# Kernel optimization log

Hardware: AMD Instinct MI355X
Metric: run time of the kernel (lower is better)

The kernel has to match this reference:

```python
import jax, jax.numpy as jnp
import numpy as np

N_NODES = 50000
N_EDGES = 1600000
IN_CH = 128
HEADS = 4
HEAD_DIM = 32  # out_channels // heads = 128 // 4
NEG_SLOPE = 0.2


def setup_inputs() -> dict:
    key = jax.random.key(0)
    ks = jax.random.split(key, 6)
    x = jax.random.normal(ks[0], (N_NODES, IN_CH), dtype=jnp.float32)
    edge_index = jax.random.randint(ks[1], (2, N_EDGES), 0, N_NODES, dtype=jnp.int64)
    W = jax.random.normal(ks[2], (IN_CH, HEADS * HEAD_DIM), dtype=jnp.float32) * 0.1
    att_src = jax.random.normal(ks[3], (HEADS, HEAD_DIM), dtype=jnp.float32) * 0.1
    att_dst = jax.random.normal(ks[4], (HEADS, HEAD_DIM), dtype=jnp.float32) * 0.1
    bias = jax.random.normal(ks[5], (HEADS * HEAD_DIM,), dtype=jnp.float32) * 0.1
    return {"x": x, "edge_index": edge_index, "W": W,
            "att_src": att_src, "att_dst": att_dst, "bias": bias}


def reference(x, edge_index, W, att_src, att_dst, bias):
    N = x.shape[0]
    # linear projection, split heads: [N, H, C]
    h = (x @ W).reshape(N, HEADS, HEAD_DIM)
    # per-node attention logits: [N, H]
    a_src = jnp.einsum('nhc,hc->nh', h, att_src)
    a_dst = jnp.einsum('nhc,hc->nh', h, att_dst)
    # add self loops (PyG default)
    loops = jnp.arange(N, dtype=edge_index.dtype)
    src = jnp.concatenate([edge_index[0], loops])  # message source j
    dst = jnp.concatenate([edge_index[1], loops])  # message target i
    # edge attention scores: [E_total, H]
    alpha = jax.nn.leaky_relu(a_src[src] + a_dst[dst], NEG_SLOPE)
    # segment softmax over incoming edges per destination node
    amax = jax.ops.segment_max(alpha, dst, num_segments=N)
    alpha = jnp.exp(alpha - amax[dst])
    denom = jax.ops.segment_sum(alpha, dst, num_segments=N)
    alpha = alpha / (denom[dst] + 1e-16)
    # weighted scatter-aggregate: [N, H, C]
    msg = h[src] * alpha[:, :, None]
    out = jax.ops.segment_sum(msg, dst, num_segments=N)
    out = out.reshape(N, HEADS * HEAD_DIM) + bias
    return jax.nn.elu(out)
```

## Files before the change

### kernel.cpp

```cpp
#include <hip/hip_runtime.h>

typedef unsigned short u16;
typedef unsigned int u32;

#define CH 128
#define NHEAD 4
#define NEG_SLOPE 0.2f
#define ROWS_PER_BLOCK 32

#define LOG_NPB 7
#define NPB 128
#define NBMAX 400
#define BCAP 6144
#define KMAX 24
#define GPAD 16
#define BINA_BLOCKS 256

static __device__ __forceinline__ float bitf(u32 i) {
    float f; __builtin_memcpy(&f, &i, 4); return f;
}
static __device__ __forceinline__ float bflo(u32 v) { return bitf(v << 16); }
static __device__ __forceinline__ float bfhi(u32 v) { return bitf(v & 0xffff0000u); }
static __device__ __forceinline__ u16 f2bf(float f) {
    u32 i; __builtin_memcpy(&i, &f, 4);
    return (u16)((i + 0x7fffu + ((i >> 16) & 1u)) >> 16);
}
static __device__ __forceinline__ float lrelu(float v) { return v > 0.f ? v : NEG_SLOPE * v; }

static __device__ __forceinline__ int ei_at(const int* __restrict__ ei, int mode32, size_t idx) {
    return mode32 ? ei[idx] : ei[2 * idx];
}

__global__ __launch_bounds__(256) void gemmbin_kernel(
    const float* __restrict__ x, const float* __restrict__ W,
    const float* __restrict__ att_src, const float* __restrict__ att_dst,
    u16* __restrict__ h, float* __restrict__ asrc, float* __restrict__ adst, int N,
    const int* __restrict__ ei, int* __restrict__ gcur, u32* __restrict__ rec,
    int E, int NB)
{
    __shared__ float xs[ROWS_PER_BLOCK][CH];
    __shared__ u32 Wbf[CH][CH / 2];

    const int tid = threadIdx.x;

    if (blockIdx.x < BINA_BLOCKS) {
        int* hist  = (int*)&xs[0][0];
        int* hbase = hist + NBMAX;
        int* hcur  = hbase + NBMAX;
        const int mode32 = __syncthreads_or(ei[2 * tid + 1] != 0);
        for (int b = tid; b < NB; b += 256) { hist[b] = 0; hcur[b] = 0; }
        __syncthreads();
        const int chunk = (E + BINA_BLOCKS - 1) / BINA_BLOCKS;
        const int beg0 = blockIdx.x * chunk;
        const int end0 = min(E, beg0 + chunk);
#pragma unroll 4
        for (int e = beg0 + tid; e < end0; e += 256) {
            int dj = ei_at(ei, mode32, (size_t)E + e);
            atomicAdd(&hist[dj >> LOG_NPB], 1);
        }
        __syncthreads();
        for (int b = tid; b < NB; b += 256) {
            int c = hist[b];
            hbase[b] = c ? atomicAdd(&gcur[b * GPAD], c) : 0;
        }
        __syncthreads();
#pragma unroll 4
        for (int e = beg0 + tid; e < end0; e += 256) {
            int dj = ei_at(ei, mode32, (size_t)E + e);
            int sj = ei_at(ei, mode32, (size_t)e);
            int bkt = dj >> LOG_NPB;
            int r = atomicAdd(&hcur[bkt], 1);
            int pos = hbase[bkt] + r;
            if (pos < BCAP)
                rec[(size_t)bkt * BCAP + pos] = ((u32)sj << LOG_NPB) | (u32)(dj & (NPB - 1));
        }
        return;
    }

    const int gb = blockIdx.x - BINA_BLOCKS;
    const int r0b = gb * ROWS_PER_BLOCK;
    {
#pragma unroll
        for (int i = 0; i < 16; ++i) {
            int f = tid + i * 256;
            int row = f >> 5;
            int col = (f & 31) * 4;
            float4 w4 = *(const float4*)(W + (size_t)row * CH + col);
            Wbf[row][(col >> 1)]     = (u32)f2bf(w4.x) | ((u32)f2bf(w4.y) << 16);
            Wbf[row][(col >> 1) + 1] = (u32)f2bf(w4.z) | ((u32)f2bf(w4.w) << 16);
        }
#pragma unroll
        for (int i = 0; i < 4; ++i) {
            int f = tid + i * 256;
            int row = f >> 5;
            int col = (f & 31) * 4;
            if (r0b + row < N)
                *(float4*)&xs[row][col] = *(const float4*)(x + (size_t)(r0b + row) * CH + col);
        }
    }
    __syncthreads();

    const int lane = tid & 63;
    const int wave = tid >> 6;
    const int c0 = lane * 2;
    const int head = lane >> 4;
    const float as0 = att_src[c0], as1 = att_src[c0 + 1];
    const float ad0 = att_dst[c0], ad1 = att_dst[c0 + 1];
    const int rw = wave * 8;

    float acc[8][2];
#pragma unroll
    for (int r = 0; r < 8; ++r) { acc[r][0] = 0.f; acc[r][1] = 0.f; }

#pragma unroll 4
    for (int k4 = 0; k4 < 32; ++k4) {
        const int k = k4 * 4;
        u32 p0 = Wbf[k + 0][lane];
        u32 p1 = Wbf[k + 1][lane];
        u32 p2 = Wbf[k + 2][lane];
        u32 p3 = Wbf[k + 3][lane];
        float w00 = bflo(p0), w01 = bfhi(p0);
        float w10 = bflo(p1), w11 = bfhi(p1);
        float w20 = bflo(p2), w21 = bfhi(p2);
        float w30 = bflo(p3), w31 = bfhi(p3);
#pragma unroll
        for (int r = 0; r < 8; ++r) {
            float4 xv = *(const float4*)&xs[rw + r][k];
            acc[r][0] = fmaf(xv.x, w00, acc[r][0]);
            acc[r][1] = fmaf(xv.x, w01, acc[r][1]);
            acc[r][0] = fmaf(xv.y, w10, acc[r][0]);
            acc[r][1] = fmaf(xv.y, w11, acc[r][1]);
            acc[r][0] = fmaf(xv.z, w20, acc[r][0]);
            acc[r][1] = fmaf(xv.z, w21, acc[r][1]);
            acc[r][0] = fmaf(xv.w, w30, acc[r][0]);
            acc[r][1] = fmaf(xv.w, w31, acc[r][1]);
        }
    }
#pragma unroll
    for (int r = 0; r < 8; ++r) {
        int row = r0b + rw + r;
        float sdot = acc[r][0] * as0 + acc[r][1] * as1;
        float ddot = acc[r][0] * ad0 + acc[r][1] * ad1;
#pragma unroll
        for (int o = 1; o < 16; o <<= 1) {
            sdot += __shfl_xor(sdot, o, 64);
            ddot += __shfl_xor(ddot, o, 64);
        }
        if (row < N) {
            u32 hp = (u32)f2bf(acc[r][0]) | ((u32)f2bf(acc[r][1]) << 16);
            *(u32*)(h + (size_t)row * CH + c0) = hp;
            if ((lane & 15) == 0) {
                asrc[row * NHEAD + head] = sdot;
                adst[row * NHEAD + head] = ddot;
            }
        }
    }
}

__global__ __launch_bounds__(256) void binB_kernel(
    const int* __restrict__ gcur, const u32* __restrict__ rec,
    int* __restrict__ csr, int* __restrict__ begA, int* __restrict__ degA, int N)
{
    __shared__ int outb[BCAP];
    __shared__ int lcnt[NPB];
    __shared__ int lsc[NPB];
    __shared__ int lcur[NPB];
    const int tid = threadIdx.x;
    const int bkt = blockIdx.x;
    int cnt0 = gcur[bkt * GPAD];
    cnt0 = cnt0 < BCAP ? cnt0 : BCAP;
    const size_t rbase = (size_t)bkt * BCAP;

    if (tid < NPB) { lcnt[tid] = 0; lcur[tid] = 0; }

    u32 rc[KMAX];
#pragma unroll
    for (int k = 0; k < KMAX; ++k) {
        int i = tid + k * 256;
        rc[k] = (i < cnt0) ? rec[rbase + i] : 0xffffffffu;
    }
    __syncthreads();
#pragma unroll
    for (int k = 0; k < KMAX; ++k)
        if (rc[k] != 0xffffffffu) atomicAdd(&lcnt[rc[k] & (NPB - 1)], 1);
    __syncthreads();
    if (tid < NPB) lsc[tid] = lcnt[tid];
    __syncthreads();
    for (int o = 1; o < NPB; o <<= 1) {
        int v = (tid < NPB && tid >= o) ? lsc[tid - o] : 0;
        __syncthreads();
        if (tid < NPB) lsc[tid] += v;
        __syncthreads();
    }
#pragma unroll
    for (int k = 0; k < KMAX; ++k) {
        if (rc[k] != 0xffffffffu) {
            int local = rc[k] & (NPB - 1);
            int r = atomicAdd(&lcur[local], 1);
            int slot = (lsc[local] - lcnt[local]) + r;
            outb[slot] = (int)(rc[k] >> LOG_NPB);
        }
    }
    __syncthreads();
    for (int i = tid; i < cnt0; i += 256)
        csr[rbase + i] = outb[i];
    if (tid < NPB) {
        int node = (bkt << LOG_NPB) + tid;
        if (node < N) {
            begA[node] = (int)rbase + (lsc[tid] - lcnt[tid]);
            degA[node] = lcnt[tid];
        }
    }
}

__global__ __launch_bounds__(256) void agg_kernel(
    const u16* __restrict__ h, const float* __restrict__ asrc, const float* __restrict__ adst,
    const int* __restrict__ begA, const int* __restrict__ degA, const int* __restrict__ csr,
    const float* __restrict__ bias, float* __restrict__ out, int N)
{
    const int lane = threadIdx.x & 63;
    const int wave = threadIdx.x >> 6;
    const int node = blockIdx.x * 4 + wave;
    if (node >= N) return;
    const int g = lane >> 4;
    const int l = lane & 15;
    const int c8 = l * 8;
    const int head = l >> 2;
    const int beg = begA[node];
    const int end = beg + degA[node];
    const float4 ad4 = *(const float4*)(adst + node * 4);
    const float adh = (head == 0) ? ad4.x : (head == 1) ? ad4.y : (head == 2) ? ad4.z : ad4.w;
    const float4 asl = *(const float4*)(asrc + node * 4);
    const float aslh = (head == 0) ? asl.x : (head == 1) ? asl.y : (head == 2) ? asl.z : asl.w;
    const float mh = lrelu(aslh + adh);

    float acc[8];
#pragma unroll
    for (int k = 0; k < 8; ++k) acc[k] = 0.f;
    float s = 0.f;

    int e = beg + g;
    if (e < end) {
        int j0 = csr[e];
        int j1 = csr[e + 4];
        bool v1 = (e + 4) < end;
        j0 = ((u32)j0 < (u32)N) ? j0 : 0;
        j1 = ((u32)j1 < (u32)N) ? j1 : 0;
        float a0 = asrc[j0 * NHEAD + head];
        float a1 = asrc[j1 * NHEAD + head];
        a1 = v1 ? a1 : -1e30f;
        uint4 h0 = *(const uint4*)(h + (size_t)j0 * CH + c8);
        uint4 h1 = *(const uint4*)(h + (size_t)j1 * CH + c8);
        for (;;) {
            const int ep = e + 8;
            bool vp0 = ep < end;
            bool vp1 = (ep + 4) < end;
            int jp0 = csr[ep];
            int jp1 = csr[ep + 4];
            jp0 = ((u32)jp0 < (u32)N) ? jp0 : 0;
            jp1 = ((u32)jp1 < (u32)N) ? jp1 : 0;
            float ap0 = asrc[jp0 * NHEAD + head];
            float ap1 = asrc[jp1 * NHEAD + head];
            ap0 = vp0 ? ap0 : -1e30f;
            ap1 = vp1 ? ap1 : -1e30f;
            uint4 hp0 = *(const uint4*)(h + (size_t)jp0 * CH + c8);
            uint4 hp1 = *(const uint4*)(h + (size_t)jp1 * CH + c8);

            float w0 = __expf(lrelu(a0 + adh) - mh);
            float w1 = __expf(lrelu(a1 + adh) - mh);
            s += w0 + w1;
            acc[0] = fmaf(w0, bflo(h0.x), acc[0]);
            acc[1] = fmaf(w0, bfhi(h0.x), acc[1]);
            acc[2] = fmaf(w0, bflo(h0.y), acc[2]);
            acc[3] = fmaf(w0, bfhi(h0.y), acc[3]);
            acc[4] = fmaf(w0, bflo(h0.z), acc[4]);
            acc[5] = fmaf(w0, bfhi(h0.z), acc[5]);
            acc[6] = fmaf(w0, bflo(h0.w), acc[6]);
            acc[7] = fmaf(w0, bfhi(h0.w), acc[7]);
            acc[0] = fmaf(w1, bflo(h1.x), acc[0]);
            acc[1] = fmaf(w1, bfhi(h1.x), acc[1]);
            acc[2] = fmaf(w1, bflo(h1.y), acc[2]);
            acc[3] = fmaf(w1, bfhi(h1.y), acc[3]);
            acc[4] = fmaf(w1, bflo(h1.z), acc[4]);
            acc[5] = fmaf(w1, bfhi(h1.z), acc[5]);
            acc[6] = fmaf(w1, bflo(h1.w), acc[6]);
            acc[7] = fmaf(w1, bfhi(h1.w), acc[7]);

            a0 = ap0; a1 = ap1; h0 = hp0; h1 = hp1; e = ep;
            if (e >= end) break;
        }
    }
    if (g == 0) {
        s += 1.0f;
        uint4 hv = *(const uint4*)(h + (size_t)node * CH + c8);
        acc[0] += bflo(hv.x);
        acc[1] += bfhi(hv.x);
        acc[2] += bflo(hv.y);
        acc[3] += bfhi(hv.y);
        acc[4] += bflo(hv.z);
        acc[5] += bfhi(hv.z);
        acc[6] += bflo(hv.w);
        acc[7] += bfhi(hv.w);
    }
#pragma unroll
    for (int o = 16; o < 64; o <<= 1) {
        s += __shfl_xor(s, o, 64);
#pragma unroll
        for (int k = 0; k < 8; ++k) acc[k] += __shfl_xor(acc[k], o, 64);
    }
    if (g == 0) {
        const float inv = 1.f / (s + 1e-16f);
        float o0[8];
#pragma unroll
        for (int k = 0; k < 8; ++k) {
            float v = acc[k] * inv + bias[c8 + k];
            o0[k] = v > 0.f ? v : __expf(v) - 1.f;
        }
        float4 lo = make_float4(o0[0], o0[1], o0[2], o0[3]);
        float4 hi = make_float4(o0[4], o0[5], o0[6], o0[7]);
        *(float4*)(out + (size_t)node * CH + c8) = lo;
        *(float4*)(out + (size_t)node * CH + c8 + 4) = hi;
    }
}

extern "C" void kernel_launch(void* const* d_in, const int* in_sizes, int n_in,
                              void* d_out, int out_size, void* d_ws, size_t ws_size,
                              hipStream_t stream)
{
    const float* x       = (const float*)d_in[0];
    const int*   ei      = (const int*)d_in[1];
    const float* W       = (const float*)d_in[2];
    const float* att_src = (const float*)d_in[3];
    const float* att_dst = (const float*)d_in[4];
    const float* bias    = (const float*)d_in[5];
    float* out = (float*)d_out;
    const int N = in_sizes[0] / CH;
    const int E = in_sizes[1] / 2;
    const int NB = (N + NPB - 1) / NPB;

    char* p = (char*)d_ws;
    auto alloc = [&](size_t bytes) { char* r = p; p += (bytes + 255) & ~(size_t)255; return r; };
    u16*   h    = (u16*)alloc((size_t)N * CH * 2);
    float* asrc = (float*)alloc((size_t)N * NHEAD * 4);
    float* adst = (float*)alloc((size_t)N * NHEAD * 4);
    int*   gcur = (int*)alloc((size_t)NB * GPAD * 4);
    u32*   rec  = (u32*)alloc((size_t)NB * BCAP * 4);
    int*   csr  = (int*)alloc((size_t)NB * BCAP * 4 + 256);
    int*   begA = (int*)alloc((size_t)N * 4);
    int*   degA = (int*)alloc((size_t)N * 4);

    const int gemmBlocks = (N + ROWS_PER_BLOCK - 1) / ROWS_PER_BLOCK;
    hipMemsetAsync(gcur, 0, (size_t)NB * GPAD * 4, stream);
    gemmbin_kernel<<<BINA_BLOCKS + gemmBlocks, 256, 0, stream>>>(
        x, W, att_src, att_dst, h, asrc, adst, N, ei, gcur, rec, E, NB);
    binB_kernel<<<NB, 256, 0, stream>>>(gcur, rec, csr, begA, degA, N);
    agg_kernel<<<(N + 3) / 4, 256, 0, stream>>>(h, asrc, adst, begA, degA, csr, bias, out, N);
}
```

Before: 197.5 us.

## Read x directly from global in GEMM and deepen gather prefetch to four edges

The GEMM part no longer stages the x tile in shared memory. Each wave reads its rows straight from global memory through per-row pointers, with a scalar row base and the row index clamped to N-1. This cuts LDS use and a barrier's worth of staging, at the cost of repeated global and L1 loads of x. The aggregation loop now keeps four edges in flight per thread instead of two, with double buffering of the gathered h rows and logits to hide gather latency, which raises register use.

```diff
diff --git a/kernel.cpp b/kernel.cpp
--- a/kernel.cpp
+++ b/kernel.cpp
@@ -38,13 +38,12 @@
     const int* __restrict__ ei, int* __restrict__ gcur, u32* __restrict__ rec,
     int E, int NB)
 {
-    __shared__ float xs[ROWS_PER_BLOCK][CH];
     __shared__ u32 Wbf[CH][CH / 2];
 
     const int tid = threadIdx.x;
 
     if (blockIdx.x < BINA_BLOCKS) {
-        int* hist  = (int*)&xs[0][0];
+        int* hist  = (int*)&Wbf[0][0];
         int* hbase = hist + NBMAX;
         int* hcur  = hbase + NBMAX;
         const int mode32 = __syncthreads_or(ei[2 * tid + 1] != 0);
@@ -79,24 +78,14 @@
 
     const int gb = blockIdx.x - BINA_BLOCKS;
     const int r0b = gb * ROWS_PER_BLOCK;
-    {
-#pragma unroll
-        for (int i = 0; i < 16; ++i) {
-            int f = tid + i * 256;
-            int row = f >> 5;
-            int col = (f & 31) * 4;
-            float4 w4 = *(const float4*)(W + (size_t)row * CH + col);
-            Wbf[row][(col >> 1)]     = (u32)f2bf(w4.x) | ((u32)f2bf(w4.y) << 16);
-            Wbf[row][(col >> 1) + 1] = (u32)f2bf(w4.z) | ((u32)f2bf(w4.w) << 16);
-        }
-#pragma unroll
-        for (int i = 0; i < 4; ++i) {
-            int f = tid + i * 256;
-            int row = f >> 5;
-            int col = (f & 31) * 4;
-            if (r0b + row < N)
-                *(float4*)&xs[row][col] = *(const float4*)(x + (size_t)(r0b + row) * CH + col);
-        }
+#pragma unroll
+    for (int i = 0; i < 16; ++i) {
+        int f = tid + i * 256;
+        int row = f >> 5;
+        int col = (f & 31) * 4;
+        float4 w4 = *(const float4*)(W + (size_t)row * CH + col);
+        Wbf[row][(col >> 1)]     = (u32)f2bf(w4.x) | ((u32)f2bf(w4.y) << 16);
+        Wbf[row][(col >> 1) + 1] = (u32)f2bf(w4.z) | ((u32)f2bf(w4.w) << 16);
     }
     __syncthreads();
 
@@ -106,13 +95,21 @@
     const int head = lane >> 4;
     const float as0 = att_src[c0], as1 = att_src[c0 + 1];
     const float ad0 = att_dst[c0], ad1 = att_dst[c0 + 1];
-    const int rw = wave * 8;
+    const int rwu = __builtin_amdgcn_readfirstlane(wave * 8);
+
+    const float* xr[8];
+#pragma unroll
+    for (int r = 0; r < 8; ++r) {
+        int row = r0b + rwu + r;
+        row = row < N - 1 ? row : N - 1;
+        xr[r] = x + (size_t)row * CH;
+    }
 
     float acc[8][2];
 #pragma unroll
     for (int r = 0; r < 8; ++r) { acc[r][0] = 0.f; acc[r][1] = 0.f; }
 
-#pragma unroll 4
+#pragma unroll 2
     for (int k4 = 0; k4 < 32; ++k4) {
         const int k = k4 * 4;
         u32 p0 = Wbf[k + 0][lane];
@@ -125,7 +122,7 @@
         float w30 = bflo(p3), w31 = bfhi(p3);
 #pragma unroll
         for (int r = 0; r < 8; ++r) {
-            float4 xv = *(const float4*)&xs[rw + r][k];
+            float4 xv = *(const float4*)(xr[r] + k);
             acc[r][0] = fmaf(xv.x, w00, acc[r][0]);
             acc[r][1] = fmaf(xv.x, w01, acc[r][1]);
             acc[r][0] = fmaf(xv.y, w10, acc[r][0]);
@@ -138,7 +135,7 @@
     }
 #pragma unroll
     for (int r = 0; r < 8; ++r) {
-        int row = r0b + rw + r;
+        int row = r0b + rwu + r;
         float sdot = acc[r][0] * as0 + acc[r][1] * as1;
         float ddot = acc[r][0] * ad0 + acc[r][1] * ad1;
 #pragma unroll
@@ -241,52 +238,44 @@
 
     int e = beg + g;
     if (e < end) {
-        int j0 = csr[e];
-        int j1 = csr[e + 4];
-        bool v1 = (e + 4) < end;
-        j0 = ((u32)j0 < (u32)N) ? j0 : 0;
-        j1 = ((u32)j1 < (u32)N) ? j1 : 0;
-        float a0 = asrc[j0 * NHEAD + head];
-        float a1 = asrc[j1 * NHEAD + head];
-        a1 = v1 ? a1 : -1e30f;
-        uint4 h0 = *(const uint4*)(h + (size_t)j0 * CH + c8);
-        uint4 h1 = *(const uint4*)(h + (size_t)j1 * CH + c8);
+        uint4 hC[4]; float aC[4];
+#pragma unroll
+        for (int i = 0; i < 4; ++i) {
+            int ei = e + 4 * i;
+            int j = csr[ei];
+            j = ((u32)j < (u32)N) ? j : 0;
+            float a = asrc[j * NHEAD + head];
+            aC[i] = (ei < end) ? a : -1e30f;
+            hC[i] = *(const uint4*)(h + (size_t)j * CH + c8);
+        }
         for (;;) {
-            const int ep = e + 8;
-            bool vp0 = ep < end;
-            bool vp1 = (ep + 4) < end;
-            int jp0 = csr[ep];
-            int jp1 = csr[ep + 4];
-            jp0 = ((u32)jp0 < (u32)N) ? jp0 : 0;
-            jp1 = ((u32)jp1 < (u32)N) ? jp1 : 0;
-            float ap0 = asrc[jp0 * NHEAD + head];
-            float ap1 = asrc[jp1 * NHEAD + head];
-            ap0 = vp0 ? ap0 : -1e30f;
-            ap1 = vp1 ? ap1 : -1e30f;
-            uint4 hp0 = *(const uint4*)(h + (size_t)jp0 * CH + c8);
-            uint4 hp1 = *(const uint4*)(h + (size_t)jp1 * CH + c8);
-
-            float w0 = __expf(lrelu(a0 + adh) - mh);
-            float w1 = __expf(lrelu(a1 + adh) - mh);
-            s += w0 + w1;
-            acc[0] = fmaf(w0, bflo(h0.x), acc[0]);
-            acc[1] = fmaf(w0, bfhi(h0.x), acc[1]);
-            acc[2] = fmaf(w0, bflo(h0.y), acc[2]);
-            acc[3] = fmaf(w0, bfhi(h0.y), acc[3]);
-            acc[4] = fmaf(w0, bflo(h0.z), acc[4]);
-            acc[5] = fmaf(w0, bfhi(h0.z), acc[5]);
-            acc[6] = fmaf(w0, bflo(h0.w), acc[6]);
-            acc[7] = fmaf(w0, bfhi(h0.w), acc[7]);
-            acc[0] = fmaf(w1, bflo(h1.x), acc[0]);
-            acc[1] = fmaf(w1, bfhi(h1.x), acc[1]);
-            acc[2] = fmaf(w1, bflo(h1.y), acc[2]);
-            acc[3] = fmaf(w1, bfhi(h1.y), acc[3]);
-            acc[4] = fmaf(w1, bflo(h1.z), acc[4]);
-            acc[5] = fmaf(w1, bfhi(h1.z), acc[5]);
-            acc[6] = fmaf(w1, bflo(h1.w), acc[6]);
-            acc[7] = fmaf(w1, bfhi(h1.w), acc[7]);
-
-            a0 = ap0; a1 = ap1; h0 = hp0; h1 = hp1; e = ep;
+            const int ebase = e + 16;
+            uint4 hP[4]; float aP[4];
+#pragma unroll
+            for (int i = 0; i < 4; ++i) {
+                int ei = ebase + 4 * i;
+                int j = csr[ei];
+                j = ((u32)j < (u32)N) ? j : 0;
+                float a = asrc[j * NHEAD + head];
+                aP[i] = (ei < end) ? a : -1e30f;
+                hP[i] = *(const uint4*)(h + (size_t)j * CH + c8);
+            }
+#pragma unroll
+            for (int i = 0; i < 4; ++i) {
+                float w = __expf(lrelu(aC[i] + adh) - mh);
+                s += w;
+                acc[0] = fmaf(w, bflo(hC[i].x), acc[0]);
+                acc[1] = fmaf(w, bfhi(hC[i].x), acc[1]);
+                acc[2] = fmaf(w, bflo(hC[i].y), acc[2]);
+                acc[3] = fmaf(w, bfhi(hC[i].y), acc[3]);
+                acc[4] = fmaf(w, bflo(hC[i].z), acc[4]);
+                acc[5] = fmaf(w, bfhi(hC[i].z), acc[5]);
+                acc[6] = fmaf(w, bflo(hC[i].w), acc[6]);
+                acc[7] = fmaf(w, bfhi(hC[i].w), acc[7]);
+            }
+#pragma unroll
+            for (int i = 0; i < 4; ++i) { aC[i] = aP[i]; hC[i] = hP[i]; }
+            e = ebase;
             if (e >= end) break;
         }
     }
```

After: 201.9 us. 2.2% more time.
